# Kernel optimization log

Measured on AMD Instinct MI355X. Metric: run time of the kernel, lower is better.

## Reference

```python
import jax, jax.numpy as jnp
import numpy as np

B, H, W, C, T = 16, 32, 32, 384, 8
HID = int(4.0 * C)
EPS = 1e-6  # flax LayerNorm default


def setup_inputs() -> dict:
    key = jax.random.key(0)
    ks = jax.random.split(key, 8)
    w = lambda k, shape: jax.random.normal(k, shape, jnp.float32) * 0.02
    return {
        "x": jax.random.normal(ks[0], (B, H, W, C), jnp.float32),
        "norm1_scale": jnp.ones((C,), jnp.float32),
        "norm1_bias": jnp.zeros((C,), jnp.float32),
        "Wu": w(ks[1], (C, C)),   # CSSM input projection
        "bu": jnp.zeros((C,), jnp.float32),
        "Wg": w(ks[2], (C, C)),   # CSSM gate projection
        "bg": jnp.zeros((C,), jnp.float32),
        "A": w(ks[3], (C, C)),    # dense state-mixing matrix (dense_mixing=True)
        "norm2_scale": jnp.ones((C,), jnp.float32),
        "norm2_bias": jnp.zeros((C,), jnp.float32),
        "mlp_w1": w(ks[4], (C, HID)),
        "mlp_b1": jnp.zeros((HID,), jnp.float32),
        "mlp_w2": w(ks[5], (HID, C)),
        "mlp_b2": jnp.zeros((C,), jnp.float32),
    }


def _ln(x, scale, bias):
    mu = jnp.mean(x, axis=-1, keepdims=True)
    var = jnp.mean(jnp.square(x - mu), axis=-1, keepdims=True)
    return (x - mu) * jax.lax.rsqrt(var + EPS) * scale + bias


def reference(x, norm1_scale, norm1_bias, Wu, bu, Wg, bg, A,
              norm2_scale, norm2_bias, mlp_w1, mlp_b1, mlp_w2, mlp_b2):
    # ---- CSSM mixer branch (replaces attention) ----
    xn = _ln(x, norm1_scale, norm1_bias)                      # (B,H,W,C)
    # Input is repeated across the T timesteps, so the per-step drive u and
    # gate g are identical each step; compute them once instead of on a
    # materialized (B,T,H,W,C) video (same math as repeat + per-step proj).
    u = jnp.einsum('bhwc,cd->bhwd', xn, Wu) + bu              # (B,H,W,C)
    g = jax.nn.sigmoid(jnp.einsum('bhwc,cd->bhwd', xn, Wg) + bg)

    def step(h, _):
        # gated state-space recurrence with dense channel mixing
        h = g * jnp.einsum('bhwc,cd->bhwd', h, A) + (1.0 - g) * u
        return h, None

    h_last, _ = jax.lax.scan(step, jnp.zeros_like(u), None, length=T)
    x = x + h_last                                            # residual 1

    # ---- MLP branch ----
    xn2 = _ln(x, norm2_scale, norm2_bias)
    m = jax.nn.gelu(jnp.einsum('bhwc,cf->bhwf', xn2, mlp_w1) + mlp_b1)
    m = jnp.einsum('bhwf,fc->bhwc', m, mlp_w2) + mlp_b2
    return x + m                                              # residual 2
```

## Files before the change

kernel.cpp:

```cpp
#include <hip/hip_runtime.h>
#include <hip/hip_bf16.h>
#include <hip/hip_fp8.h>


#define CCH   384
#define SBB   400
#define NPIX  16384
#define BMROWS 64
#define NTHR  768
#define LNEPS 1e-6f
#define HBUF  (BMROWS * SBB)
#define WSC   64.0f
#define ASC   8.0f
#define DQ    0.001953125f
#define SCL1  0x7F7F7F7Fu

typedef __attribute__((ext_vector_type(4))) float f4_t;
typedef __attribute__((ext_vector_type(8))) int   i32x8;

#define OFF_WU 0u
#define OFF_WG 147456u
#define OFF_A  294912u
#define OFF_W1 442368u
#define OFF_W2 1032192u

__device__ __forceinline__ unsigned char f2e4(float f) {
  __hip_fp8_e4m3 t(f);
  return (unsigned char)t.__x;
}

#if __has_builtin(__builtin_amdgcn_cvt_pk_fp8_f32)
__device__ __forceinline__ unsigned pk4e4(float a, float b, float c, float d) {
  int v = __builtin_amdgcn_cvt_pk_fp8_f32(a, b, 0, false);
  v = __builtin_amdgcn_cvt_pk_fp8_f32(c, d, v, true);
  return (unsigned)v;
}
#else
__device__ __forceinline__ unsigned pk4e4(float a, float b, float c, float d) {
  return (unsigned)f2e4(a) | ((unsigned)f2e4(b) << 8)
       | ((unsigned)f2e4(c) << 16) | ((unsigned)f2e4(d) << 24);
}
#endif

__device__ __forceinline__ unsigned short f2bf(float f) {
  return __builtin_bit_cast(unsigned short, __float2bfloat16(f));
}
__device__ __forceinline__ unsigned pack2(float lo, float hi) {
  return (unsigned)f2bf(lo) | ((unsigned)f2bf(hi) << 16);
}
__device__ __forceinline__ float ulo(unsigned u) {
  union { unsigned x; float f; } v; v.x = u << 16; return v.f;
}
__device__ __forceinline__ float uhi(unsigned u) {
  union { unsigned x; float f; } v; v.x = u & 0xffff0000u; return v.f;
}
__device__ __forceinline__ float fsigmoid(float z) {
  return __builtin_amdgcn_rcpf(1.f + exp2f(z * -1.44269504088896f));
}

__global__ void pack_all(const float* __restrict__ Wu, const float* __restrict__ Wg,
                         const float* __restrict__ A,  const float* __restrict__ W1,
                         const float* __restrict__ W2, unsigned char* __restrict__ P) {
  const int gid = blockIdx.x * blockDim.x + threadIdx.x;
  const int l = gid & 63;
  int tile = gid >> 6;
  const float* W; int N; unsigned off; int t;
  if      (tile <  72) { W = Wu; N = 384;  off = OFF_WU; t = tile;       }
  else if (tile < 144) { W = Wg; N = 384;  off = OFF_WG; t = tile - 72;  }
  else if (tile < 216) { W = A;  N = 384;  off = OFF_A;  t = tile - 144; }
  else if (tile < 504) { W = W1; N = 1536; off = OFF_W1; t = tile - 216; }
  else if (tile < 792) { W = W2; N = 384;  off = OFF_W2; t = tile - 504; }
  else return;
  const int ntn = N >> 4;
  const int kb  = t / ntn, n16 = t % ntn;
  const int krow = kb * 128 + ((l >> 4) << 5);
  const int col  = n16 * 16 + (l & 15);
  unsigned pk[8];
  #pragma unroll
  for (int d = 0; d < 8; ++d) {
    unsigned v = 0;
    #pragma unroll
    for (int j = 0; j < 4; ++j)
      v |= (unsigned)f2e4(W[(size_t)(krow + d * 4 + j) * N + col] * WSC) << (8 * j);
    pk[d] = v;
  }
  unsigned* dst = reinterpret_cast<unsigned*>(P + off + ((size_t)t << 11) + (l << 5));
  #pragma unroll
  for (int d = 0; d < 8; ++d) dst[d] = pk[d];
}

template <int NKB>
__device__ __forceinline__ void gemm_acc(const unsigned char* sb,
                                         const unsigned char* __restrict__ wt,
                                         int kb0, int ntn, int n16base,
                                         int lane, f4_t acc[4][2]) {
  const int r    = lane & 15;
  const int koff = (lane >> 4) << 5;
  __builtin_amdgcn_s_setprio(1);
  #pragma unroll 1
  for (int kb = 0; kb < NKB; ++kb) {
    const int ac = kb * 128 + koff;
    i32x8 p[4];
    #pragma unroll
    for (int pt = 0; pt < 4; ++pt)
      p[pt] = *reinterpret_cast<const i32x8*>(&sb[(pt * 16 + r) * SBB + ac]);
    const unsigned char* bt =
        wt + (((size_t)((kb0 + kb) * ntn + n16base)) << 11) + (lane << 5);
    #pragma unroll
    for (int ct = 0; ct < 2; ++ct) {
      const i32x8 w = *reinterpret_cast<const i32x8*>(bt + (ct << 11));
      #pragma unroll
      for (int pt = 0; pt < 4; ++pt)
        acc[pt][ct] = __builtin_amdgcn_mfma_scale_f32_16x16x128_f8f6f4(
            w, p[pt], acc[pt][ct], 0 , 0 ,
            0, (int)SCL1, 0, (int)SCL1);
    }
  }
  __builtin_amdgcn_s_setprio(0);
}

__device__ __forceinline__ void write_tile(unsigned char* sb, const f4_t t[4][2],
                                           int ch0, int lane) {
  const int pixb = lane & 15;
  #pragma unroll
  for (int pt = 0; pt < 4; ++pt) {
    const int pix = pt * 16 + pixb;
    #pragma unroll
    for (int ct = 0; ct < 2; ++ct) {
      const unsigned v = pk4e4(t[pt][ct][0] * ASC, t[pt][ct][1] * ASC,
                               t[pt][ct][2] * ASC, t[pt][ct][3] * ASC);
      *reinterpret_cast<unsigned*>(&sb[pix * SBB + ch0 + ct * 16]) = v;
    }
  }
}

__device__ __forceinline__ void zero_acc(f4_t a[4][2]) {
  #pragma unroll
  for (int pt = 0; pt < 4; ++pt)
    #pragma unroll
    for (int ct = 0; ct < 2; ++ct) a[pt][ct] = (f4_t){0.f, 0.f, 0.f, 0.f};
}

__global__ __launch_bounds__(NTHR, 1) void cssm_main(
    const float* __restrict__ x,
    const float* __restrict__ n1s, const float* __restrict__ n1b,
    const float* __restrict__ bu, const float* __restrict__ bg,
    const float* __restrict__ n2s, const float* __restrict__ n2b,
    const float* __restrict__ b1, const float* __restrict__ b2,
    const unsigned char* __restrict__ wp,
    float* __restrict__ out) {
  __shared__ unsigned char sm[3 * HBUF];
  __shared__ float part[BMROWS][12][2];
  __shared__ float srow[BMROWS][2];
  unsigned char* bA = sm;
  unsigned char* bB = sm + HBUF;
  unsigned char* bC = sm + 2 * HBUF;

  const int tid = threadIdx.x;
  const int lane = tid & 63;
  const int nw = tid >> 6;
  const int r0 = blockIdx.x * BMROWS;
  const int pixb = lane & 15;
  const int ch0  = nw * 32 + ((lane >> 4) << 2);

  if (tid < 512) {
    const int row = tid >> 3, seg = tid & 7;
    const float* xr = x + (size_t)(r0 + row) * CCH + seg * 48;
    float v[48];
    float s = 0.f, s2 = 0.f;
    #pragma unroll
    for (int i = 0; i < 12; ++i) {
      const f4_t t = reinterpret_cast<const f4_t*>(xr)[i];
      #pragma unroll
      for (int j = 0; j < 4; ++j) { const float f = t[j]; v[i * 4 + j] = f; s += f; s2 += f * f; }
    }
    #pragma unroll
    for (int o = 1; o < 8; o <<= 1) { s += __shfl_xor(s, o, 64); s2 += __shfl_xor(s2, o, 64); }
    const float mu = s * (1.f / CCH);
    const float rs = rsqrtf(fmaxf(s2 * (1.f / CCH) - mu * mu, 0.f) + LNEPS);
    #pragma unroll
    for (int g8 = 0; g8 < 6; ++g8) {
      float w[8];
      #pragma unroll
      for (int j = 0; j < 8; ++j) {
        const int colc = seg * 48 + g8 * 8 + j;
        w[j] = ((v[g8 * 8 + j] - mu) * rs * n1s[colc] + n1b[colc]) * ASC;
      }
      uint2 pk;
      pk.x = pk4e4(w[0], w[1], w[2], w[3]);
      pk.y = pk4e4(w[4], w[5], w[6], w[7]);
      *reinterpret_cast<uint2*>(&bA[row * SBB + seg * 48 + g8 * 8]) = pk;
    }
  }
  __syncthreads();

  f4_t acc[4][2];
  unsigned gp[4][2][2], cp[4][2][2];
  zero_acc(acc);
  gemm_acc<3>(bA, wp + OFF_WG, 0, 24, nw * 2, lane, acc);
  #pragma unroll
  for (int ct = 0; ct < 2; ++ct) {
    const f4_t bgq = *reinterpret_cast<const f4_t*>(&bg[ch0 + ct * 16]);
    #pragma unroll
    for (int pt = 0; pt < 4; ++pt) {
      gp[pt][ct][0] = pack2(fsigmoid(acc[pt][ct][0] * DQ + bgq[0]),
                            fsigmoid(acc[pt][ct][1] * DQ + bgq[1]));
      gp[pt][ct][1] = pack2(fsigmoid(acc[pt][ct][2] * DQ + bgq[2]),
                            fsigmoid(acc[pt][ct][3] * DQ + bgq[3]));
    }
  }
  zero_acc(acc);
  gemm_acc<3>(bA, wp + OFF_WU, 0, 24, nw * 2, lane, acc);
  #pragma unroll
  for (int ct = 0; ct < 2; ++ct) {
    const f4_t buq = *reinterpret_cast<const f4_t*>(&bu[ch0 + ct * 16]);
    #pragma unroll
    for (int pt = 0; pt < 4; ++pt) {
      #pragma unroll
      for (int p = 0; p < 2; ++p) {
        const unsigned g = gp[pt][ct][p];
        const float c0 = (1.f - ulo(g)) * (acc[pt][ct][2 * p]     * DQ + buq[2 * p]);
        const float c1 = (1.f - uhi(g)) * (acc[pt][ct][2 * p + 1] * DQ + buq[2 * p + 1]);
        acc[pt][ct][2 * p] = c0; acc[pt][ct][2 * p + 1] = c1;
        cp[pt][ct][p] = pack2(c0, c1);
        gp[pt][ct][p] = pack2(ulo(g) * DQ, uhi(g) * DQ);
      }
    }
  }
  write_tile(bB, acc, ch0, lane);
  __syncthreads();

  {
    unsigned char* cur = bB;
    unsigned char* alt = bA;
    #pragma unroll 1
    for (int stp = 0; stp < 7; ++stp) {
      zero_acc(acc);
      gemm_acc<3>(cur, wp + OFF_A, 0, 24, nw * 2, lane, acc);
      #pragma unroll
      for (int pt = 0; pt < 4; ++pt)
        #pragma unroll
        for (int ct = 0; ct < 2; ++ct)
          #pragma unroll
          for (int p = 0; p < 2; ++p) {
            const unsigned g = gp[pt][ct][p], c = cp[pt][ct][p];
            acc[pt][ct][2 * p]     = ulo(g) * acc[pt][ct][2 * p]     + ulo(c);
            acc[pt][ct][2 * p + 1] = uhi(g) * acc[pt][ct][2 * p + 1] + uhi(c);
          }
      if (stp < 6) {
        write_tile(alt, acc, ch0, lane);
        unsigned char* t = cur; cur = alt; alt = t;
        __syncthreads();
      }
    }
  }

  #pragma unroll
  for (int pt = 0; pt < 4; ++pt) {
    const int pix = pt * 16 + pixb;
    float s = 0.f, s2 = 0.f;
    #pragma unroll
    for (int ct = 0; ct < 2; ++ct) {
      const size_t pos = (size_t)(r0 + pix) * CCH + ch0 + ct * 16;
      const f4_t xq = *reinterpret_cast<const f4_t*>(&x[pos]);
      f4_t yq;
      #pragma unroll
      for (int j = 0; j < 4; ++j) {
        const float y = xq[j] + acc[pt][ct][j];
        yq[j] = y; acc[pt][ct][j] = y;
        s += y; s2 += y * y;
      }
      *reinterpret_cast<f4_t*>(&out[pos]) = yq;
    }
    s += __shfl_xor(s, 16, 64); s2 += __shfl_xor(s2, 16, 64);
    s += __shfl_xor(s, 32, 64); s2 += __shfl_xor(s2, 32, 64);
    if (lane < 16) { part[pix][nw][0] = s; part[pix][nw][1] = s2; }
  }
  __syncthreads();
  if (tid < BMROWS) {
    float s = 0.f, s2 = 0.f;
    #pragma unroll
    for (int w = 0; w < 12; ++w) { s += part[tid][w][0]; s2 += part[tid][w][1]; }
    const float mu = s * (1.f / CCH);
    srow[tid][0] = mu;
    srow[tid][1] = rsqrtf(fmaxf(s2 * (1.f / CCH) - mu * mu, 0.f) + LNEPS);
  }
  __syncthreads();
  {
    f4_t scq[2], bsq[2];
    #pragma unroll
    for (int ct = 0; ct < 2; ++ct) {
      scq[ct] = *reinterpret_cast<const f4_t*>(&n2s[ch0 + ct * 16]);
      bsq[ct] = *reinterpret_cast<const f4_t*>(&n2b[ch0 + ct * 16]);
    }
    #pragma unroll
    for (int pt = 0; pt < 4; ++pt) {
      const int pix = pt * 16 + pixb;
      const float mu = srow[pix][0], rs = srow[pix][1];
      #pragma unroll
      for (int ct = 0; ct < 2; ++ct)
        #pragma unroll
        for (int j = 0; j < 4; ++j)
          acc[pt][ct][j] = (acc[pt][ct][j] - mu) * rs * scq[ct][j] + bsq[ct][j];
    }
    write_tile(bA, acc, ch0, lane);
  }
  __syncthreads();

  f4_t aco[4][2];
  zero_acc(aco);
  #pragma unroll 1
  for (int ch = 0; ch < 4; ++ch) {
    unsigned char* buf = (ch & 1) ? bC : bB;
    zero_acc(acc);
    gemm_acc<3>(bA, wp + OFF_W1, 0, 96, ch * 24 + nw * 2, lane, acc);
    #pragma unroll
    for (int ct = 0; ct < 2; ++ct) {
      const f4_t b1q = *reinterpret_cast<const f4_t*>(&b1[ch * 384 + ch0 + ct * 16]);
      #pragma unroll
      for (int pt = 0; pt < 4; ++pt)
        #pragma unroll
        for (int j = 0; j < 4; ++j) {
          const float z = acc[pt][ct][j] * DQ + b1q[j];
          const float m = z * z;
          const float t = z * fmaf(m, 0.044715f, 1.0f);
          const float e = exp2f(t * -2.30211774f);
          acc[pt][ct][j] = z * __builtin_amdgcn_rcpf(1.f + e);
        }
    }
    write_tile(buf, acc, ch0, lane);
    __syncthreads();
    gemm_acc<3>(buf, wp + OFF_W2, ch * 3, 24, nw * 2, lane, aco);
  }

  {
    f4_t b2q[2];
    #pragma unroll
    for (int ct = 0; ct < 2; ++ct)
      b2q[ct] = *reinterpret_cast<const f4_t*>(&b2[ch0 + ct * 16]);
    #pragma unroll
    for (int pt = 0; pt < 4; ++pt) {
      const int pix = pt * 16 + pixb;
      #pragma unroll
      for (int ct = 0; ct < 2; ++ct) {
        const size_t pos = (size_t)(r0 + pix) * CCH + ch0 + ct * 16;
        const f4_t yq = *reinterpret_cast<const f4_t*>(&out[pos]);
        f4_t o;
        #pragma unroll
        for (int j = 0; j < 4; ++j)
          o[j] = yq[j] + aco[pt][ct][j] * DQ + b2q[ct][j];
        *reinterpret_cast<f4_t*>(&out[pos]) = o;
      }
    }
  }
}

extern "C" void kernel_launch(void* const* d_in, const int* in_sizes, int n_in,
                              void* d_out, int out_size, void* d_ws, size_t ws_size,
                              hipStream_t stream) {
  const float* x   = (const float*)d_in[0];
  const float* n1s = (const float*)d_in[1];
  const float* n1b = (const float*)d_in[2];
  const float* Wu  = (const float*)d_in[3];
  const float* bu  = (const float*)d_in[4];
  const float* Wg  = (const float*)d_in[5];
  const float* bg  = (const float*)d_in[6];
  const float* A   = (const float*)d_in[7];
  const float* n2s = (const float*)d_in[8];
  const float* n2b = (const float*)d_in[9];
  const float* W1  = (const float*)d_in[10];
  const float* b1  = (const float*)d_in[11];
  const float* W2  = (const float*)d_in[12];
  const float* b2  = (const float*)d_in[13];
  unsigned char* wp = (unsigned char*)d_ws;
  float* out = (float*)d_out;

  pack_all<<<(792 * 64) / 256, 256, 0, stream>>>(Wu, Wg, A, W1, W2, wp);

  cssm_main<<<NPIX / BMROWS, NTHR, 0, stream>>>(
      x, n1s, n1b, bu, bg, n2s, n2b, b1, b2, wp, out);
}
```

Before: 76.10 us.

## Keep gate/drive in fp32 registers, fold fp8 scaling, raise waves per EU

Replaces the bf16-packed gate and drive registers with fp32 vectors and folds the ASC activation scale into the stored values, so write_tile no longer multiplies and the recurrence works in scaled units (rescaled by IASC at the residual). The LDS row stride changes from 400 to 432 bytes, likely to alter bank conflict patterns. The launch bound drops the min-blocks hint and adds amdgpu_waves_per_eu(3), which asks the compiler to cap registers for higher occupancy. LDS use per block (~83KB) may still limit residency, and more fp32 state raises register pressure and spill risk.

Result: no change. 75.38 us (-0.9%).

```diff
diff --git a/kernel.cpp b/kernel.cpp
--- a/kernel.cpp
+++ b/kernel.cpp
@@ -4,7 +4,7 @@
 
 
 #define CCH   384
-#define SBB   400
+#define SBB   432
 #define NPIX  16384
 #define BMROWS 64
 #define NTHR  768
@@ -12,6 +12,8 @@
 #define HBUF  (BMROWS * SBB)
 #define WSC   64.0f
 #define ASC   8.0f
+#define IASC  0.125f
+#define GSC   0.015625f
 #define DQ    0.001953125f
 #define SCL1  0x7F7F7F7Fu
 
@@ -42,18 +44,6 @@
 }
 #endif
 
-__device__ __forceinline__ unsigned short f2bf(float f) {
-  return __builtin_bit_cast(unsigned short, __float2bfloat16(f));
-}
-__device__ __forceinline__ unsigned pack2(float lo, float hi) {
-  return (unsigned)f2bf(lo) | ((unsigned)f2bf(hi) << 16);
-}
-__device__ __forceinline__ float ulo(unsigned u) {
-  union { unsigned x; float f; } v; v.x = u << 16; return v.f;
-}
-__device__ __forceinline__ float uhi(unsigned u) {
-  union { unsigned x; float f; } v; v.x = u & 0xffff0000u; return v.f;
-}
 __device__ __forceinline__ float fsigmoid(float z) {
   return __builtin_amdgcn_rcpf(1.f + exp2f(z * -1.44269504088896f));
 }
@@ -127,8 +117,8 @@
     const int pix = pt * 16 + pixb;
     #pragma unroll
     for (int ct = 0; ct < 2; ++ct) {
-      const unsigned v = pk4e4(t[pt][ct][0] * ASC, t[pt][ct][1] * ASC,
-                               t[pt][ct][2] * ASC, t[pt][ct][3] * ASC);
+      const unsigned v = pk4e4(t[pt][ct][0], t[pt][ct][1],
+                               t[pt][ct][2], t[pt][ct][3]);
       *reinterpret_cast<unsigned*>(&sb[pix * SBB + ch0 + ct * 16]) = v;
     }
   }
@@ -141,7 +131,9 @@
     for (int ct = 0; ct < 2; ++ct) a[pt][ct] = (f4_t){0.f, 0.f, 0.f, 0.f};
 }
 
-__global__ __launch_bounds__(NTHR, 1) void cssm_main(
+__global__ __launch_bounds__(NTHR)
+__attribute__((amdgpu_waves_per_eu(3)))
+void cssm_main(
     const float* __restrict__ x,
     const float* __restrict__ n1s, const float* __restrict__ n1b,
     const float* __restrict__ bu, const float* __restrict__ bg,
@@ -194,20 +186,17 @@
   }
   __syncthreads();
 
-  f4_t acc[4][2];
-  unsigned gp[4][2][2], cp[4][2][2];
+  f4_t acc[4][2], gf[4][2], cf[4][2];
   zero_acc(acc);
   gemm_acc<3>(bA, wp + OFF_WG, 0, 24, nw * 2, lane, acc);
   #pragma unroll
   for (int ct = 0; ct < 2; ++ct) {
     const f4_t bgq = *reinterpret_cast<const f4_t*>(&bg[ch0 + ct * 16]);
     #pragma unroll
-    for (int pt = 0; pt < 4; ++pt) {
-      gp[pt][ct][0] = pack2(fsigmoid(acc[pt][ct][0] * DQ + bgq[0]),
-                            fsigmoid(acc[pt][ct][1] * DQ + bgq[1]));
-      gp[pt][ct][1] = pack2(fsigmoid(acc[pt][ct][2] * DQ + bgq[2]),
-                            fsigmoid(acc[pt][ct][3] * DQ + bgq[3]));
-    }
+    for (int pt = 0; pt < 4; ++pt)
+      #pragma unroll
+      for (int j = 0; j < 4; ++j)
+        gf[pt][ct][j] = fsigmoid(acc[pt][ct][j] * DQ + bgq[j]);
   }
   zero_acc(acc);
   gemm_acc<3>(bA, wp + OFF_WU, 0, 24, nw * 2, lane, acc);
@@ -215,19 +204,15 @@
   for (int ct = 0; ct < 2; ++ct) {
     const f4_t buq = *reinterpret_cast<const f4_t*>(&bu[ch0 + ct * 16]);
     #pragma unroll
-    for (int pt = 0; pt < 4; ++pt) {
-      #pragma unroll
-      for (int p = 0; p < 2; ++p) {
-        const unsigned g = gp[pt][ct][p];
-        const float c0 = (1.f - ulo(g)) * (acc[pt][ct][2 * p]     * DQ + buq[2 * p]);
-        const float c1 = (1.f - uhi(g)) * (acc[pt][ct][2 * p + 1] * DQ + buq[2 * p + 1]);
-        acc[pt][ct][2 * p] = c0; acc[pt][ct][2 * p + 1] = c1;
-        cp[pt][ct][p] = pack2(c0, c1);
-        gp[pt][ct][p] = pack2(ulo(g) * DQ, uhi(g) * DQ);
-      }
-    }
-  }
-  write_tile(bB, acc, ch0, lane);
+    for (int pt = 0; pt < 4; ++pt)
+      #pragma unroll
+      for (int j = 0; j < 4; ++j) {
+        const float g = gf[pt][ct][j];
+        cf[pt][ct][j] = (1.f - g) * (acc[pt][ct][j] * DQ + buq[j]) * ASC;
+        gf[pt][ct][j] = g * GSC;
+      }
+  }
+  write_tile(bB, cf, ch0, lane);
   __syncthreads();
 
   {
@@ -242,11 +227,8 @@
         #pragma unroll
         for (int ct = 0; ct < 2; ++ct)
           #pragma unroll
-          for (int p = 0; p < 2; ++p) {
-            const unsigned g = gp[pt][ct][p], c = cp[pt][ct][p];
-            acc[pt][ct][2 * p]     = ulo(g) * acc[pt][ct][2 * p]     + ulo(c);
-            acc[pt][ct][2 * p + 1] = uhi(g) * acc[pt][ct][2 * p + 1] + uhi(c);
-          }
+          for (int j = 0; j < 4; ++j)
+            acc[pt][ct][j] = gf[pt][ct][j] * acc[pt][ct][j] + cf[pt][ct][j];
       if (stp < 6) {
         write_tile(alt, acc, ch0, lane);
         unsigned char* t = cur; cur = alt; alt = t;
@@ -266,7 +248,7 @@
       f4_t yq;
       #pragma unroll
       for (int j = 0; j < 4; ++j) {
-        const float y = xq[j] + acc[pt][ct][j];
+        const float y = xq[j] + acc[pt][ct][j] * IASC;
         yq[j] = y; acc[pt][ct][j] = y;
         s += y; s2 += y * y;
       }
@@ -290,8 +272,10 @@
     f4_t scq[2], bsq[2];
     #pragma unroll
     for (int ct = 0; ct < 2; ++ct) {
-      scq[ct] = *reinterpret_cast<const f4_t*>(&n2s[ch0 + ct * 16]);
-      bsq[ct] = *reinterpret_cast<const f4_t*>(&n2b[ch0 + ct * 16]);
+      const f4_t sc = *reinterpret_cast<const f4_t*>(&n2s[ch0 + ct * 16]);
+      const f4_t bs = *reinterpret_cast<const f4_t*>(&n2b[ch0 + ct * 16]);
+      #pragma unroll
+      for (int j = 0; j < 4; ++j) { scq[ct][j] = sc[j] * ASC; bsq[ct][j] = bs[j] * ASC; }
     }
     #pragma unroll
     for (int pt = 0; pt < 4; ++pt) {
@@ -325,7 +309,7 @@
           const float m = z * z;
           const float t = z * fmaf(m, 0.044715f, 1.0f);
           const float e = exp2f(t * -2.30211774f);
-          acc[pt][ct][j] = z * __builtin_amdgcn_rcpf(1.f + e);
+          acc[pt][ct][j] = (z * ASC) * __builtin_amdgcn_rcpf(1.f + e);
         }
     }
     write_tile(buf, acc, ch0, lane);
```

## Keep recurrence matrix A in registers and fold fp8 scaling into constants

Applied to the files above, without the earlier changes.

Each wave now loads its slice of the state-mixing matrix A into registers once and reuses it across all 7 recurrence steps, so A is no longer re-read from global memory every step. The fp8 activation scale is folded into the recurrence constants (gate, drive), the LN2 scale/bias and the GELU output, which removes the per-element multiply inside write_tile. The shared-memory row stride grows from 400 to 432 bytes, presumably to change LDS bank mapping. Launch bounds are relaxed and a waves_per_eu hint is added, which trades register budget against occupancy while A now occupies extra registers.

Measured after the change: 85.29 us. 12.1% more time.

```diff
diff --git a/kernel.cpp b/kernel.cpp
--- a/kernel.cpp
+++ b/kernel.cpp
@@ -4,7 +4,7 @@
 
 
 #define CCH   384
-#define SBB   400
+#define SBB   432
 #define NPIX  16384
 #define BMROWS 64
 #define NTHR  768
@@ -12,6 +12,8 @@
 #define HBUF  (BMROWS * SBB)
 #define WSC   64.0f
 #define ASC   8.0f
+#define IASC  0.125f
+#define GSC   0.015625f
 #define DQ    0.001953125f
 #define SCL1  0x7F7F7F7Fu
 
@@ -119,6 +121,29 @@
   __builtin_amdgcn_s_setprio(0);
 }
 
+__device__ __forceinline__ void gemm_rec(const unsigned char* sb,
+                                         const i32x8 (&wA)[3][2],
+                                         int lane, f4_t acc[4][2]) {
+  const int r    = lane & 15;
+  const int koff = (lane >> 4) << 5;
+  __builtin_amdgcn_s_setprio(1);
+  #pragma unroll
+  for (int kb = 0; kb < 3; ++kb) {
+    const int ac = kb * 128 + koff;
+    i32x8 p[4];
+    #pragma unroll
+    for (int pt = 0; pt < 4; ++pt)
+      p[pt] = *reinterpret_cast<const i32x8*>(&sb[(pt * 16 + r) * SBB + ac]);
+    #pragma unroll
+    for (int ct = 0; ct < 2; ++ct)
+      #pragma unroll
+      for (int pt = 0; pt < 4; ++pt)
+        acc[pt][ct] = __builtin_amdgcn_mfma_scale_f32_16x16x128_f8f6f4(
+            wA[kb][ct], p[pt], acc[pt][ct], 0, 0, 0, (int)SCL1, 0, (int)SCL1);
+  }
+  __builtin_amdgcn_s_setprio(0);
+}
+
 __device__ __forceinline__ void write_tile(unsigned char* sb, const f4_t t[4][2],
                                            int ch0, int lane) {
   const int pixb = lane & 15;
@@ -127,8 +152,8 @@
     const int pix = pt * 16 + pixb;
     #pragma unroll
     for (int ct = 0; ct < 2; ++ct) {
-      const unsigned v = pk4e4(t[pt][ct][0] * ASC, t[pt][ct][1] * ASC,
-                               t[pt][ct][2] * ASC, t[pt][ct][3] * ASC);
+      const unsigned v = pk4e4(t[pt][ct][0], t[pt][ct][1],
+                               t[pt][ct][2], t[pt][ct][3]);
       *reinterpret_cast<unsigned*>(&sb[pix * SBB + ch0 + ct * 16]) = v;
     }
   }
@@ -141,7 +166,9 @@
     for (int ct = 0; ct < 2; ++ct) a[pt][ct] = (f4_t){0.f, 0.f, 0.f, 0.f};
 }
 
-__global__ __launch_bounds__(NTHR, 1) void cssm_main(
+__global__ __launch_bounds__(NTHR)
+__attribute__((amdgpu_waves_per_eu(3)))
+void cssm_main(
     const float* __restrict__ x,
     const float* __restrict__ n1s, const float* __restrict__ n1b,
     const float* __restrict__ bu, const float* __restrict__ bg,
@@ -211,23 +238,36 @@
   }
   zero_acc(acc);
   gemm_acc<3>(bA, wp + OFF_WU, 0, 24, nw * 2, lane, acc);
-  #pragma unroll
-  for (int ct = 0; ct < 2; ++ct) {
-    const f4_t buq = *reinterpret_cast<const f4_t*>(&bu[ch0 + ct * 16]);
-    #pragma unroll
-    for (int pt = 0; pt < 4; ++pt) {
-      #pragma unroll
-      for (int p = 0; p < 2; ++p) {
-        const unsigned g = gp[pt][ct][p];
-        const float c0 = (1.f - ulo(g)) * (acc[pt][ct][2 * p]     * DQ + buq[2 * p]);
-        const float c1 = (1.f - uhi(g)) * (acc[pt][ct][2 * p + 1] * DQ + buq[2 * p + 1]);
-        acc[pt][ct][2 * p] = c0; acc[pt][ct][2 * p + 1] = c1;
-        cp[pt][ct][p] = pack2(c0, c1);
-        gp[pt][ct][p] = pack2(ulo(g) * DQ, uhi(g) * DQ);
+  {
+    f4_t cf[4][2];
+    #pragma unroll
+    for (int ct = 0; ct < 2; ++ct) {
+      const f4_t buq = *reinterpret_cast<const f4_t*>(&bu[ch0 + ct * 16]);
+      #pragma unroll
+      for (int pt = 0; pt < 4; ++pt) {
+        #pragma unroll
+        for (int p = 0; p < 2; ++p) {
+          const unsigned g = gp[pt][ct][p];
+          const float c0 = (1.f - ulo(g)) * (acc[pt][ct][2 * p]     * DQ + buq[2 * p]) * ASC;
+          const float c1 = (1.f - uhi(g)) * (acc[pt][ct][2 * p + 1] * DQ + buq[2 * p + 1]) * ASC;
+          cf[pt][ct][2 * p] = c0; cf[pt][ct][2 * p + 1] = c1;
+          cp[pt][ct][p] = pack2(c0, c1);
+          gp[pt][ct][p] = pack2(ulo(g) * GSC, uhi(g) * GSC);
+        }
       }
     }
-  }
-  write_tile(bB, acc, ch0, lane);
+    write_tile(bB, cf, ch0, lane);
+  }
+
+  i32x8 wA[3][2];
+  {
+    const unsigned char* ab = wp + OFF_A + ((size_t)(nw * 2) << 11) + (lane << 5);
+    #pragma unroll
+    for (int kb = 0; kb < 3; ++kb)
+      #pragma unroll
+      for (int ct = 0; ct < 2; ++ct)
+        wA[kb][ct] = *reinterpret_cast<const i32x8*>(ab + ((size_t)(kb * 24 + ct) << 11));
+  }
   __syncthreads();
 
   {
@@ -236,7 +276,7 @@
     #pragma unroll 1
     for (int stp = 0; stp < 7; ++stp) {
       zero_acc(acc);
-      gemm_acc<3>(cur, wp + OFF_A, 0, 24, nw * 2, lane, acc);
+      gemm_rec(cur, wA, lane, acc);
       #pragma unroll
       for (int pt = 0; pt < 4; ++pt)
         #pragma unroll
@@ -266,7 +306,7 @@
       f4_t yq;
       #pragma unroll
       for (int j = 0; j < 4; ++j) {
-        const float y = xq[j] + acc[pt][ct][j];
+        const float y = xq[j] + acc[pt][ct][j] * IASC;
         yq[j] = y; acc[pt][ct][j] = y;
         s += y; s2 += y * y;
       }
@@ -290,8 +330,10 @@
     f4_t scq[2], bsq[2];
     #pragma unroll
     for (int ct = 0; ct < 2; ++ct) {
-      scq[ct] = *reinterpret_cast<const f4_t*>(&n2s[ch0 + ct * 16]);
-      bsq[ct] = *reinterpret_cast<const f4_t*>(&n2b[ch0 + ct * 16]);
+      const f4_t sc = *reinterpret_cast<const f4_t*>(&n2s[ch0 + ct * 16]);
+      const f4_t bs = *reinterpret_cast<const f4_t*>(&n2b[ch0 + ct * 16]);
+      #pragma unroll
+      for (int j = 0; j < 4; ++j) { scq[ct][j] = sc[j] * ASC; bsq[ct][j] = bs[j] * ASC; }
     }
     #pragma unroll
     for (int pt = 0; pt < 4; ++pt) {
@@ -325,7 +367,7 @@
           const float m = z * z;
           const float t = z * fmaf(m, 0.044715f, 1.0f);
           const float e = exp2f(t * -2.30211774f);
-          acc[pt][ct][j] = z * __builtin_amdgcn_rcpf(1.f + e);
+          acc[pt][ct][j] = (z * ASC) * __builtin_amdgcn_rcpf(1.f + e);
         }
     }
     write_tile(buf, acc, ch0, lane);
```
